# Kernel tuning notes

Measured on AMD Instinct MI355X. Metric: run time of the kernel, lower is better.

## Reference

```python
import jax, jax.numpy as jnp
import numpy as np

D_MODEL = 1024
MAX_BIRTHS = 4
BIRTH_THRESHOLD = 0.45


def setup_inputs() -> dict:
    key = jax.random.key(0)
    ks = jax.random.split(key, 5)
    B, Tu, Tm, D = 4, 4096, 2048, D_MODEL
    return {
        "o_micro": jax.random.normal(ks[0], (B, Tu, D), jnp.float32),
        "o_macro": jax.random.normal(ks[1], (B, Tm, D), jnp.float32),
        "r_emer_acc": jax.random.uniform(ks[2], (B, Tu, Tm), jnp.float32),
        "chunk_size": 128,
        # vesica_field: Linear(2D -> D, no bias); torch weight layout (D, 2D)
        "W_vesica": jax.random.normal(ks[3], (D, 2 * D), jnp.float32) * (1.0 / np.sqrt(2.0 * D)),
        # birth_gate: Linear(D -> 1)
        "w_gate": jax.random.normal(ks[4], (D,), jnp.float32) * (1.0 / np.sqrt(float(D))),
        "b_gate": jnp.zeros((), jnp.float32),
        "threshold_bias": jnp.zeros((), jnp.float32),
    }


def reference(o_micro, o_macro, r_emer_acc, chunk_size, W_vesica, w_gate, b_gate, threshold_bias):
    B, Tu, D = o_micro.shape
    # accumulated resonance per micro token: mean over macro dim -> (B, Tu)
    micro_res = r_emer_acc.mean(axis=-1)
    # adjacent-pair resonance -> (B, Tu-1)
    pair_res = (micro_res[:, :-1] + micro_res[:, 1:]) * 0.5
    threshold = BIRTH_THRESHOLD + jnp.tanh(threshold_bias) * 0.2
    above = pair_res > threshold
    pair_scores = pair_res * above.astype(pair_res.dtype)
    k = MAX_BIRTHS  # min(max_births, Tu-1); Tu >> max_births here
    topk_vals, topk_idx = jax.lax.top_k(pair_scores, k)  # (B, k)
    birth_mask = topk_vals > 0
    n_births = birth_mask.sum()
    # gather parent pairs -> (B, k, D) each
    left = jnp.take_along_axis(o_micro, topk_idx[..., None], axis=1)
    right = jnp.take_along_axis(o_micro, (topk_idx + 1)[..., None], axis=1)
    combined = jnp.concatenate([left, right], axis=-1)  # (B, k, 2D)
    child = jnp.einsum("bkf,df->bkd", combined, W_vesica)
    gate = jax.nn.sigmoid(jnp.einsum("bkd,d->bk", child, w_gate) + b_gate)
    child = child * gate[..., None] * birth_mask[..., None].astype(child.dtype)
    # compact born children to the front (stable), zeros pad the tail —
    # identical to the torch ragged stack+pad given fixed width k
    order = jnp.argsort(~birth_mask, axis=1, stable=True)  # (B, k)
    child = jnp.take_along_axis(child, order[..., None], axis=1)
    o_macro_expanded = jnp.concatenate([o_macro, child], axis=1)  # (B, Tm+k, D)
    return o_macro_expanded, n_births
```

## Files before the change

### kernel.cpp

```cpp
#include <hip/hip_runtime.h>
#include <math.h>

#define BATCH 4
#define TU 4096
#define TM 2048
#define DM 1024
#define FF 2048
#define KB 4
#define NROWS (BATCH*KB)
#define OUT_TM (TM+KB)

__global__ __launch_bounds__(256) void k_mean_copy(
    const float* __restrict__ r_emer, const float* __restrict__ o_macro,
    float* __restrict__ micro_res, float* __restrict__ out)
{
    const int tid  = threadIdx.x;
    const int lane = tid & 63;
    const int wave = tid >> 6;
    const int row  = blockIdx.x * 4 + wave;

    const float4* rp = (const float4*)(r_emer + (size_t)row * FF);
    float s = 0.0f;
    #pragma unroll
    for (int j = 0; j < 8; ++j) {
        float4 v = rp[lane + 64 * j];
        s += v.x + v.y + v.z + v.w;
    }
    #pragma unroll
    for (int off = 32; off >= 1; off >>= 1)
        s += __shfl_down(s, off, 64);
    if (lane == 0) micro_res[row] = s * (1.0f / 2048.0f);

    const float4* src = (const float4*)o_macro;
    float4* dst = (float4*)out;
    const int NF4       = BATCH * TM * DM / 4;
    const int PER_BATCH = TM * DM / 4;
    const int DST_BATCH = OUT_TM * DM / 4;
    for (int e = blockIdx.x * 256 + tid; e < NF4; e += gridDim.x * 256) {
        int b = e >> 19;
        int q = e & (PER_BATCH - 1);
        dst[b * DST_BATCH + q] = src[e];
    }
}

__global__ __launch_bounds__(256) void k_topk(
    const float* __restrict__ micro_res,
    const float* __restrict__ threshold_bias,
    int* __restrict__ topk_idx, float* __restrict__ topk_val)
{
    __shared__ float res[TU];
    __shared__ float rv[256];
    __shared__ int   ri[256];
    __shared__ int   sel[KB];
    __shared__ float selv[KB];

    const int b = blockIdx.x, tid = threadIdx.x;
    const float* mr = micro_res + b * TU;
    for (int i = tid; i < TU; i += 256) res[i] = mr[i];
    __syncthreads();

    const float thr = 0.45f + tanhf(threshold_bias[0]) * 0.2f;

    for (int p = 0; p < KB; ++p) {
        float bv = -1.0f; int bi = 0x7fffffff;
        for (int t = tid; t < TU - 1; t += 256) {
            bool skip = false;
            for (int q = 0; q < p; ++q) if (sel[q] == t) skip = true;
            if (skip) continue;
            float pr = (res[t] + res[t + 1]) * 0.5f;
            float sc = pr > thr ? pr : 0.0f;
            if (sc > bv || (sc == bv && t < bi)) { bv = sc; bi = t; }
        }
        rv[tid] = bv; ri[tid] = bi;
        __syncthreads();
        for (int s = 128; s >= 1; s >>= 1) {
            if (tid < s) {
                float ov = rv[tid + s]; int oi = ri[tid + s];
                if (ov > rv[tid] || (ov == rv[tid] && oi < ri[tid])) {
                    rv[tid] = ov; ri[tid] = oi;
                }
            }
            __syncthreads();
        }
        if (tid == 0) { sel[p] = ri[0]; selv[p] = rv[0]; }
        __syncthreads();
    }
    if (tid < KB) {
        topk_idx[b * KB + tid] = sel[tid];
        topk_val[b * KB + tid] = selv[tid];
    }
}

__global__ __launch_bounds__(256) void k_child(
    const float* __restrict__ o_micro, const float* __restrict__ W,
    const int* __restrict__ topk_idx, float* __restrict__ child_raw)
{
    const int d   = blockIdx.x;
    const int tid = threadIdx.x;
    const int lane = tid & 63;
    const int wave = tid >> 6;
    const int f0  = tid * 8;

    __shared__ int sidx[NROWS];
    if (tid < NROWS) sidx[tid] = topk_idx[tid];
    __syncthreads();

    const float4* wp = (const float4*)(W + (size_t)d * FF + f0);
    const float4 w0 = wp[0], w1 = wp[1];

    float acc[NROWS];
    #pragma unroll
    for (int r = 0; r < NROWS; ++r) {
        const int bb  = r >> 2;
        const int idx = sidx[r];
        const float* srcrow;
        int fo;
        if (f0 < DM) { srcrow = o_micro + ((size_t)bb * TU + idx) * DM;     fo = f0; }
        else         { srcrow = o_micro + ((size_t)bb * TU + idx + 1) * DM; fo = f0 - DM; }
        const float4* cp = (const float4*)(srcrow + fo);
        float4 c0 = cp[0], c1 = cp[1];
        acc[r] = c0.x * w0.x + c0.y * w0.y + c0.z * w0.z + c0.w * w0.w
               + c1.x * w1.x + c1.y * w1.y + c1.z * w1.z + c1.w * w1.w;
    }

    #pragma unroll
    for (int r = 0; r < NROWS; ++r) {
        float v = acc[r];
        #pragma unroll
        for (int off = 32; off >= 1; off >>= 1)
            v += __shfl_down(v, off, 64);
        acc[r] = v;
    }
    __shared__ float part[4][NROWS];
    if (lane == 0) {
        #pragma unroll
        for (int r = 0; r < NROWS; ++r) part[wave][r] = acc[r];
    }
    __syncthreads();
    if (tid < NROWS)
        child_raw[(size_t)tid * DM + d] =
            part[0][tid] + part[1][tid] + part[2][tid] + part[3][tid];
}

__global__ __launch_bounds__(256) void k_gate(
    const float* __restrict__ child_raw, const float* __restrict__ w_gate,
    const float* __restrict__ b_gate, const float* __restrict__ topk_val,
    float* __restrict__ out)
{
    const int row = blockIdx.x;
    const int b = row >> 2, k = row & 3;
    const int tid = threadIdx.x;
    const int lane = tid & 63, wave = tid >> 6;

    const float4* cp = (const float4*)(child_raw + (size_t)row * DM);
    const float4* wp = (const float4*)w_gate;
    float4 c = cp[tid], w = wp[tid];
    float dotp = c.x * w.x + c.y * w.y + c.z * w.z + c.w * w.w;

    #pragma unroll
    for (int off = 32; off >= 1; off >>= 1)
        dotp += __shfl_down(dotp, off, 64);

    __shared__ float ps[4];
    __shared__ float scale_s;
    if (lane == 0) ps[wave] = dotp;
    __syncthreads();
    if (tid == 0) {
        float dsum = ps[0] + ps[1] + ps[2] + ps[3] + b_gate[0];
        float gate = 1.0f / (1.0f + expf(-dsum));
        float mask = topk_val[row] > 0.0f ? 1.0f : 0.0f;
        scale_s = gate * mask;
    }
    __syncthreads();

    const float s = scale_s;
    float4 o; o.x = c.x * s; o.y = c.y * s; o.z = c.z * s; o.w = c.w * s;
    float4* op = (float4*)(out + ((size_t)b * OUT_TM + TM + k) * DM);
    op[tid] = o;

    if (row == 0 && tid == 0) {
        int n = 0;
        for (int i = 0; i < NROWS; ++i) n += (topk_val[i] > 0.0f) ? 1 : 0;
        out[(size_t)BATCH * OUT_TM * DM] = (float)n;
    }
}

extern "C" void kernel_launch(void* const* d_in, const int* in_sizes, int n_in,
                              void* d_out, int out_size, void* d_ws, size_t ws_size,
                              hipStream_t stream) {
    const float* o_micro   = (const float*)d_in[0];
    const float* o_macro   = (const float*)d_in[1];
    const float* r_emer    = (const float*)d_in[2];
    const float* W_vesica  = (const float*)d_in[4];
    const float* w_gate    = (const float*)d_in[5];
    const float* b_gate    = (const float*)d_in[6];
    const float* thr_bias  = (const float*)d_in[7];
    float* out = (float*)d_out;

    float* wsf       = (float*)d_ws;
    float* micro_res = wsf;
    int*   topk_idx  = (int*)(wsf + 16384);
    float* topk_val  = wsf + 16400;
    float* child_raw = wsf + 16416;

    k_mean_copy<<<4096, 256, 0, stream>>>(r_emer, o_macro, micro_res, out);
    k_topk<<<BATCH, 256, 0, stream>>>(micro_res, thr_bias, topk_idx, topk_val);
    k_child<<<DM, 256, 0, stream>>>(o_micro, W_vesica, topk_idx, child_raw);
    k_gate<<<NROWS, 256, 0, stream>>>(child_raw, w_gate, b_gate, topk_val, out);
}
```

Measured before the change: 303.0 us.

## Fold gate into precomputed W^T·w_gate vector and fuse gate into top-k and child kernels

The gate logit is computed algebraically as combined·(W^T w_gate). That vector u is produced by 8 extra blocks added to the bandwidth-bound mean/copy kernel, which lets the gate be evaluated inside the top-k kernel. The child kernel then applies the scale and writes straight to the output, so the separate gate kernel and the child_raw round trip go away. The mean/copy path also switches to nontemporal loads and stores, with loads issued before the copy. This changes float summation order for the gate and adds some serial work to the 4-block top-k kernel.

New measurement: 323.4 us. 6.7% more time.

```diff
diff --git a/kernel.cpp b/kernel.cpp
--- a/kernel.cpp
+++ b/kernel.cpp
@@ -10,51 +10,90 @@
 #define NROWS (BATCH*KB)
 #define OUT_TM (TM+KB)
 
-__global__ __launch_bounds__(256) void k_mean_copy(
+typedef float fv4 __attribute__((ext_vector_type(4)));
+
+__global__ __launch_bounds__(256) void k_mean_copy_u(
     const float* __restrict__ r_emer, const float* __restrict__ o_macro,
-    float* __restrict__ micro_res, float* __restrict__ out)
+    const float* __restrict__ W, const float* __restrict__ w_gate,
+    float* __restrict__ micro_res, float* __restrict__ u,
+    float* __restrict__ out)
 {
     const int tid  = threadIdx.x;
     const int lane = tid & 63;
     const int wave = tid >> 6;
-    const int row  = blockIdx.x * 4 + wave;
-
-    const float4* rp = (const float4*)(r_emer + (size_t)row * FF);
-    float s = 0.0f;
-    #pragma unroll
-    for (int j = 0; j < 8; ++j) {
-        float4 v = rp[lane + 64 * j];
-        s += v.x + v.y + v.z + v.w;
-    }
-    #pragma unroll
-    for (int off = 32; off >= 1; off >>= 1)
-        s += __shfl_down(s, off, 64);
-    if (lane == 0) micro_res[row] = s * (1.0f / 2048.0f);
-
-    const float4* src = (const float4*)o_macro;
-    float4* dst = (float4*)out;
-    const int NF4       = BATCH * TM * DM / 4;
-    const int PER_BATCH = TM * DM / 4;
-    const int DST_BATCH = OUT_TM * DM / 4;
-    for (int e = blockIdx.x * 256 + tid; e < NF4; e += gridDim.x * 256) {
-        int b = e >> 19;
-        int q = e & (PER_BATCH - 1);
-        dst[b * DST_BATCH + q] = src[e];
-    }
-}
-
-__global__ __launch_bounds__(256) void k_topk(
-    const float* __restrict__ micro_res,
-    const float* __restrict__ threshold_bias,
-    int* __restrict__ topk_idx, float* __restrict__ topk_val)
+
+    if (blockIdx.x < 4096) {
+        const int row = blockIdx.x * 4 + wave;
+        const fv4* rp = (const fv4*)(r_emer + (size_t)row * FF);
+        fv4 a[8];
+        #pragma unroll
+        for (int j = 0; j < 8; ++j)
+            a[j] = __builtin_nontemporal_load(rp + lane + 64 * j);
+
+        const fv4* src = (const fv4*)o_macro;
+        fv4* dst = (fv4*)out;
+        const int e0 = blockIdx.x * 256 + tid;
+        #pragma unroll
+        for (int it = 0; it < 2; ++it) {
+            int e = e0 + it * (4096 * 256);
+            int b = e >> 19;
+            int q = e & ((1 << 19) - 1);
+            fv4 v = __builtin_nontemporal_load(src + e);
+            __builtin_nontemporal_store(v, dst + (size_t)b * (OUT_TM * DM / 4) + q);
+        }
+
+        float s = 0.0f;
+        #pragma unroll
+        for (int j = 0; j < 8; ++j) s += a[j].x + a[j].y + a[j].z + a[j].w;
+        #pragma unroll
+        for (int off = 32; off >= 1; off >>= 1)
+            s += __shfl_down(s, off, 64);
+        if (lane == 0) micro_res[row] = s * (1.0f / 2048.0f);
+    } else {
+        const int bid = blockIdx.x - 4096;
+        const float4* W4 = (const float4*)W;
+        const int col = bid * 64 + lane;
+        float4 acc = make_float4(0.f, 0.f, 0.f, 0.f);
+        const int d0 = wave * 256;
+        for (int d = d0; d < d0 + 256; ++d) {
+            float g = w_gate[d];
+            float4 wv = W4[(size_t)d * 512 + col];
+            acc.x += g * wv.x; acc.y += g * wv.y;
+            acc.z += g * wv.z; acc.w += g * wv.w;
+        }
+        __shared__ float4 part[4][64];
+        part[wave][lane] = acc;
+        __syncthreads();
+        if (tid < 64) {
+            float4 s0 = part[0][tid], s1 = part[1][tid];
+            float4 s2 = part[2][tid], s3 = part[3][tid];
+            float4 r;
+            r.x = s0.x + s1.x + s2.x + s3.x;
+            r.y = s0.y + s1.y + s2.y + s3.y;
+            r.z = s0.z + s1.z + s2.z + s3.z;
+            r.w = s0.w + s1.w + s2.w + s3.w;
+            ((float4*)u)[bid * 64 + tid] = r;
+        }
+    }
+}
+
+__global__ __launch_bounds__(256) void k_topk_gate(
+    const float* __restrict__ micro_res, const float* __restrict__ threshold_bias,
+    const float* __restrict__ u, const float* __restrict__ o_micro,
+    const float* __restrict__ b_gate,
+    int* __restrict__ topk_idx, float* __restrict__ scale,
+    float* __restrict__ counts)
 {
     __shared__ float res[TU];
     __shared__ float rv[256];
     __shared__ int   ri[256];
     __shared__ int   sel[KB];
     __shared__ float selv[KB];
+    __shared__ float red[4];
+    __shared__ float sc[KB];
 
     const int b = blockIdx.x, tid = threadIdx.x;
+    const int lane = tid & 63, wave = tid >> 6;
     const float* mr = micro_res + b * TU;
     for (int i = tid; i < TU; i += 256) res[i] = mr[i];
     __syncthreads();
@@ -68,8 +107,8 @@
             for (int q = 0; q < p; ++q) if (sel[q] == t) skip = true;
             if (skip) continue;
             float pr = (res[t] + res[t + 1]) * 0.5f;
-            float sc = pr > thr ? pr : 0.0f;
-            if (sc > bv || (sc == bv && t < bi)) { bv = sc; bi = t; }
+            float scv = pr > thr ? pr : 0.0f;
+            if (scv > bv || (scv == bv && t < bi)) { bv = scv; bi = t; }
         }
         rv[tid] = bv; ri[tid] = bi;
         __syncthreads();
@@ -85,15 +124,49 @@
         if (tid == 0) { sel[p] = ri[0]; selv[p] = rv[0]; }
         __syncthreads();
     }
+
+    const int f0 = tid * 8;
+    const float4* up = (const float4*)(u + f0);
+    const float4 u0 = up[0], u1 = up[1];
+    for (int k = 0; k < KB; ++k) {
+        const int idx = sel[k];
+        const float* srcrow;
+        int fo;
+        if (f0 < DM) { srcrow = o_micro + ((size_t)b * TU + idx) * DM;     fo = f0; }
+        else         { srcrow = o_micro + ((size_t)b * TU + idx + 1) * DM; fo = f0 - DM; }
+        const float4* cp = (const float4*)(srcrow + fo);
+        float4 c0 = cp[0], c1 = cp[1];
+        float dsum = c0.x * u0.x + c0.y * u0.y + c0.z * u0.z + c0.w * u0.w
+                   + c1.x * u1.x + c1.y * u1.y + c1.z * u1.z + c1.w * u1.w;
+        #pragma unroll
+        for (int off = 32; off >= 1; off >>= 1)
+            dsum += __shfl_down(dsum, off, 64);
+        if (lane == 0) red[wave] = dsum;
+        __syncthreads();
+        if (tid == 0) {
+            float tot = red[0] + red[1] + red[2] + red[3] + b_gate[0];
+            float g = 1.0f / (1.0f + expf(-tot));
+            float m = selv[k] > 0.0f ? 1.0f : 0.0f;
+            sc[k] = g * m;
+        }
+        __syncthreads();
+    }
+
     if (tid < KB) {
         topk_idx[b * KB + tid] = sel[tid];
-        topk_val[b * KB + tid] = selv[tid];
-    }
-}
-
-__global__ __launch_bounds__(256) void k_child(
+        scale[b * KB + tid] = sc[tid];
+    }
+    if (tid == 0) {
+        float c = 0.f;
+        for (int k = 0; k < KB; ++k) c += (selv[k] > 0.0f) ? 1.0f : 0.0f;
+        counts[b] = c;
+    }
+}
+
+__global__ __launch_bounds__(256) void k_child_out(
     const float* __restrict__ o_micro, const float* __restrict__ W,
-    const int* __restrict__ topk_idx, float* __restrict__ child_raw)
+    const int* __restrict__ topk_idx, const float* __restrict__ scale,
+    const float* __restrict__ counts, float* __restrict__ out)
 {
     const int d   = blockIdx.x;
     const int tid = threadIdx.x;
@@ -101,8 +174,9 @@
     const int wave = tid >> 6;
     const int f0  = tid * 8;
 
-    __shared__ int sidx[NROWS];
-    if (tid < NROWS) sidx[tid] = topk_idx[tid];
+    __shared__ int   sidx[NROWS];
+    __shared__ float ssc[NROWS];
+    if (tid < NROWS) { sidx[tid] = topk_idx[tid]; ssc[tid] = scale[tid]; }
     __syncthreads();
 
     const float4* wp = (const float4*)(W + (size_t)d * FF + f0);
@@ -137,52 +211,13 @@
         for (int r = 0; r < NROWS; ++r) part[wave][r] = acc[r];
     }
     __syncthreads();
-    if (tid < NROWS)
-        child_raw[(size_t)tid * DM + d] =
-            part[0][tid] + part[1][tid] + part[2][tid] + part[3][tid];
-}
-
-__global__ __launch_bounds__(256) void k_gate(
-    const float* __restrict__ child_raw, const float* __restrict__ w_gate,
-    const float* __restrict__ b_gate, const float* __restrict__ topk_val,
-    float* __restrict__ out)
-{
-    const int row = blockIdx.x;
-    const int b = row >> 2, k = row & 3;
-    const int tid = threadIdx.x;
-    const int lane = tid & 63, wave = tid >> 6;
-
-    const float4* cp = (const float4*)(child_raw + (size_t)row * DM);
-    const float4* wp = (const float4*)w_gate;
-    float4 c = cp[tid], w = wp[tid];
-    float dotp = c.x * w.x + c.y * w.y + c.z * w.z + c.w * w.w;
-
-    #pragma unroll
-    for (int off = 32; off >= 1; off >>= 1)
-        dotp += __shfl_down(dotp, off, 64);
-
-    __shared__ float ps[4];
-    __shared__ float scale_s;
-    if (lane == 0) ps[wave] = dotp;
-    __syncthreads();
-    if (tid == 0) {
-        float dsum = ps[0] + ps[1] + ps[2] + ps[3] + b_gate[0];
-        float gate = 1.0f / (1.0f + expf(-dsum));
-        float mask = topk_val[row] > 0.0f ? 1.0f : 0.0f;
-        scale_s = gate * mask;
-    }
-    __syncthreads();
-
-    const float s = scale_s;
-    float4 o; o.x = c.x * s; o.y = c.y * s; o.z = c.z * s; o.w = c.w * s;
-    float4* op = (float4*)(out + ((size_t)b * OUT_TM + TM + k) * DM);
-    op[tid] = o;
-
-    if (row == 0 && tid == 0) {
-        int n = 0;
-        for (int i = 0; i < NROWS; ++i) n += (topk_val[i] > 0.0f) ? 1 : 0;
-        out[(size_t)BATCH * OUT_TM * DM] = (float)n;
-    }
+    if (tid < NROWS) {
+        float v = (part[0][tid] + part[1][tid] + part[2][tid] + part[3][tid]) * ssc[tid];
+        out[((size_t)(tid >> 2) * OUT_TM + TM + (tid & 3)) * DM + d] = v;
+    }
+    if (blockIdx.x == 0 && tid == 0)
+        out[(size_t)BATCH * OUT_TM * DM] =
+            counts[0] + counts[1] + counts[2] + counts[3];
 }
 
 extern "C" void kernel_launch(void* const* d_in, const int* in_sizes, int n_in,
@@ -199,12 +234,15 @@
 
     float* wsf       = (float*)d_ws;
     float* micro_res = wsf;
-    int*   topk_idx  = (int*)(wsf + 16384);
-    float* topk_val  = wsf + 16400;
-    float* child_raw = wsf + 16416;
-
-    k_mean_copy<<<4096, 256, 0, stream>>>(r_emer, o_macro, micro_res, out);
-    k_topk<<<BATCH, 256, 0, stream>>>(micro_res, thr_bias, topk_idx, topk_val);
-    k_child<<<DM, 256, 0, stream>>>(o_micro, W_vesica, topk_idx, child_raw);
-    k_gate<<<NROWS, 256, 0, stream>>>(child_raw, w_gate, b_gate, topk_val, out);
-}
+    float* u         = wsf + 16384;
+    int*   topk_idx  = (int*)(wsf + 18432);
+    float* scale     = wsf + 18448;
+    float* counts    = wsf + 18464;
+
+    k_mean_copy_u<<<4104, 256, 0, stream>>>(r_emer, o_macro, W_vesica, w_gate,
+                                            micro_res, u, out);
+    k_topk_gate<<<BATCH, 256, 0, stream>>>(micro_res, thr_bias, u, o_micro,
+                                           b_gate, topk_idx, scale, counts);
+    k_child_out<<<DM, 256, 0, stream>>>(o_micro, W_vesica, topk_idx, scale,
+                                        counts, out);
+}
```
